# Kernel tuning notes

Measured on AMD Instinct MI355X. Metric: run time of the kernel, lower is better.

Reference implementation:

```python
import jax, jax.numpy as jnp
import numpy as np

N = 20000   # nodes
E = 320000  # edges
F0 = 32     # num_features
H = 8       # GAT heads
G = 64      # graphs in batch


def setup_inputs() -> dict:
    key = jax.random.key(0)
    ks = jax.random.split(key, 16)
    def p(k, shape, s=0.05):
        return jax.random.normal(k, shape, jnp.float32) * s
    d = {}
    d['x'] = jax.random.normal(ks[0], (N, F0), jnp.float32)
    d['edge_index'] = jax.random.randint(ks[1], (2, E), 0, N, dtype=jnp.int32)
    d['edge_weights'] = jax.random.uniform(ks[2], (E,), jnp.float32)
    d['batch'] = jnp.sort(jax.random.randint(ks[3], (N,), 0, G, dtype=jnp.int32))
    # GATConv(32 -> 32, heads=8)
    d['W_gat'] = p(ks[4], (F0, H * F0)); d['att_src'] = p(ks[5], (H, F0))
    d['att_dst'] = p(ks[6], (H, F0));    d['b_gat'] = jnp.zeros((H * F0,), jnp.float32)
    # residual Linear(256 -> 1024) (widened so the residual add is shape-consistent)
    d['W_res'] = p(ks[7], (H * F0, 1024)); d['b_res'] = jnp.zeros((1024,), jnp.float32)
    # GCNConv(256 -> 512) + BN1
    d['W2'] = p(ks[8], (H * F0, 512)); d['b2'] = jnp.zeros((512,), jnp.float32)
    d['g1'] = jnp.ones((512,), jnp.float32); d['be1'] = jnp.zeros((512,), jnp.float32)
    d['m1'] = jnp.zeros((512,), jnp.float32); d['v1'] = jnp.ones((512,), jnp.float32)
    # GCNConv(512 -> 1024) + BN2
    d['W3'] = p(ks[9], (512, 1024)); d['b3'] = jnp.zeros((1024,), jnp.float32)
    d['g2'] = jnp.ones((1024,), jnp.float32); d['be2'] = jnp.zeros((1024,), jnp.float32)
    d['m2'] = jnp.zeros((1024,), jnp.float32); d['v2'] = jnp.ones((1024,), jnp.float32)
    # head
    d['Wf1'] = p(ks[10], (1024, 256)); d['bf1'] = jnp.zeros((256,), jnp.float32)
    d['Wf2'] = p(ks[11], (256, 2));    d['bf2'] = jnp.zeros((2,), jnp.float32)
    return d


def _add_self_loops(edge_index, edge_weight, n):
    loop = jnp.arange(n, dtype=edge_index.dtype)
    ei = jnp.concatenate([edge_index, jnp.stack([loop, loop])], axis=1)
    ew = jnp.concatenate([edge_weight, jnp.ones((n,), edge_weight.dtype)])
    return ei, ew


def _gat(x, edge_index, W, att_src, att_dst, b, n):
    # PyG GATConv, concat=True, eval (attention dropout off). Self-loops already added.
    src, dst = edge_index[0], edge_index[1]
    h = (x @ W).reshape(n, H, -1)                    # [N,H,C]
    a_s = jnp.einsum('nhc,hc->nh', h, att_src)        # [N,H]
    a_d = jnp.einsum('nhc,hc->nh', h, att_dst)
    e = jax.nn.leaky_relu(a_s[src] + a_d[dst], 0.2)   # [E,H]
    m = jax.ops.segment_max(e, dst, num_segments=n)   # softmax over incoming edges
    ex = jnp.exp(e - m[dst])
    s = jax.ops.segment_sum(ex, dst, num_segments=n)
    alpha = ex / s[dst]
    out = jax.ops.segment_sum(h[src] * alpha[:, :, None], dst, num_segments=n)
    return out.reshape(n, -1) + b                     # [N,H*C]


def _gcn(x, edge_index, w, W, b, n):
    # PyG GCNConv with symmetric normalization; self-loops (weight 1) already added.
    src, dst = edge_index[0], edge_index[1]
    deg = jax.ops.segment_sum(w, dst, num_segments=n)
    dinv = jnp.where(deg > 0, jax.lax.rsqrt(jnp.maximum(deg, 1e-12)), 0.0)
    norm = dinv[src] * w * dinv[dst]                  # [E]
    h = x @ W                                         # transform first (cheaper)
    return jax.ops.segment_sum(h[src] * norm[:, None], dst, num_segments=n) + b


def _bn(x, g, b, m, v):
    return g * (x - m) * jax.lax.rsqrt(v + 1e-5) + b


def reference(x, edge_index, edge_weights, batch, W_gat, att_src, att_dst, b_gat,
              W_res, b_res, W2, b2, g1, be1, m1, v1, W3, b3, g2, be2, m2, v2,
              Wf1, bf1, Wf2, bf2):
    n = x.shape[0]
    ei, ew = _add_self_loops(edge_index, edge_weights, n)
    h = jax.nn.relu(_gat(x, ei, W_gat, att_src, att_dst, b_gat, n))   # [N,256]
    res = h @ W_res + b_res                                           # [N,1024]
    h = _gcn(h, ei, ew, W2, b2, n)                                    # [N,512]
    h = jax.nn.relu(_bn(h, g1, be1, m1, v1))
    h = _gcn(h, ei, ew, W3, b3, n)                                    # [N,1024]
    h = jax.nn.relu(_bn(h, g2, be2, m2, v2))
    h = h + res
    pooled = jax.ops.segment_max(h, batch, num_segments=G)            # global max pool [G,1024]
    z = jax.nn.relu(pooled @ Wf1 + bf1)                               # dropout is eval no-op
    return z @ Wf2 + bf2                                              # [G,2]
```

## Files before the change

### kernel.cpp

```cpp
#include <hip/hip_runtime.h>
#include <hip/hip_bf16.h>

#define NN 20000
#define EE 320000
#define GG 64
#define EN (EE + NN)
#define MT 157

typedef float f32x4 __attribute__((ext_vector_type(4)));
typedef __bf16 bf16x4 __attribute__((ext_vector_type(4)));
typedef __bf16 bf16x8 __attribute__((ext_vector_type(8)));

__device__ __forceinline__ void gl_lds16(const void* g, void* l) {
    __builtin_amdgcn_global_load_lds((const __attribute__((address_space(1))) void*)g,
                                     (__attribute__((address_space(3))) void*)l, 16, 0, 0);
}

__global__ void sentinel_kernel(float* out, int n) {
    int i = blockIdx.x * 256 + threadIdx.x;
    if (i < n) out[i] = 12345.0f;
}

__global__ void init_kernel(int* deg_cnt, float* deg_w, int* fill, float* pooled) {
    int i = blockIdx.x * 256 + threadIdx.x;
    if (i < NN) { deg_cnt[i] = 1; deg_w[i] = 1.0f; fill[i] = 0; }
    if (i < GG * 1024) pooled[i] = -INFINITY;
}

__global__ void deg_kernel(const int* __restrict__ ei, const float* __restrict__ ew,
                           int* deg_cnt, float* deg_w) {
    int e = blockIdx.x * 256 + threadIdx.x;
    if (e >= EE) return;
    int dst = ei[EE + e];
    atomicAdd(&deg_cnt[dst], 1);
    atomicAdd(&deg_w[dst], ew[e]);
}

__global__ __launch_bounds__(256) void scan_kernel(const int* __restrict__ deg_cnt, int* __restrict__ rowptr) {
    __shared__ int partial[256];
    int tid = threadIdx.x;
    const int chunk = (NN + 255) / 256;
    int s0 = tid * chunk, s1 = min(s0 + chunk, NN);
    int sum = 0;
    for (int i = s0; i < s1; i++) sum += deg_cnt[i];
    partial[tid] = sum;
    __syncthreads();
    if (tid == 0) {
        int run = 0;
        for (int i = 0; i < 256; i++) { int t = partial[i]; partial[i] = run; run += t; }
        rowptr[NN] = run;
    }
    __syncthreads();
    int run = partial[tid];
    for (int i = s0; i < s1; i++) { rowptr[i] = run; run += deg_cnt[i]; }
}

__global__ void fill_kernel(const int* __restrict__ ei, const float* __restrict__ ew,
                            const float* __restrict__ deg_w, const int* __restrict__ rowptr,
                            int* fill, int* __restrict__ csr_src, float* __restrict__ csr_norm) {
    int e = blockIdx.x * 256 + threadIdx.x;
    if (e >= EN) return;
    int src, dst; float w;
    if (e < EE) { src = ei[e]; dst = ei[EE + e]; w = ew[e]; }
    else        { src = dst = e - EE; w = 1.0f; }
    int pos = atomicAdd(&fill[dst], 1);
    int slot = rowptr[dst] + pos;
    csr_src[slot] = src;
    csr_norm[slot] = rsqrtf(deg_w[src]) * w * rsqrtf(deg_w[dst]);
}

__global__ __launch_bounds__(256) void convert_all(
    const float* __restrict__ W2, const float* __restrict__ W3, const float* __restrict__ Wres,
    __bf16* __restrict__ W2t, __bf16* __restrict__ W3t, __bf16* __restrict__ Wrt)
{
    __shared__ float tile[64][65];
    int b = blockIdx.x;
    const float* W; __bf16* Wt; int K, N, bx, by;
    if (b < 32)       { W = W2;   Wt = W2t; K = 256; N = 512;  int bb = b;       bx = bb & 7;  by = bb >> 3; }
    else if (b < 160) { W = W3;   Wt = W3t; K = 512; N = 1024; int bb = b - 32;  bx = bb & 15; by = bb >> 4; }
    else              { W = Wres; Wt = Wrt; K = 256; N = 1024; int bb = b - 160; bx = bb & 15; by = bb >> 4; }
    int kb = by * 64, nb = bx * 64;
    int tx = threadIdx.x & 63, ty = threadIdx.x >> 6;
#pragma unroll
    for (int i = ty; i < 64; i += 4)
        tile[i][tx] = W[(size_t)(kb + i) * N + nb + tx];
    __syncthreads();
#pragma unroll
    for (int i = ty; i < 64; i += 4)
        Wt[(size_t)(nb + i) * K + kb + tx] = (__bf16)tile[tx][i];
}


__global__ __launch_bounds__(256) void a_compute(
    const float* __restrict__ x, const float* __restrict__ W,
    const float* __restrict__ att_s, const float* __restrict__ att_d,
    float* __restrict__ a_s, float* __restrict__ a_d)
{
    __shared__ float wss[8][32], wsd[8][32];
    __shared__ float xs[32][33];
    int tid = threadIdx.x;
    {
        int h = tid >> 5, k = tid & 31;
        float s = 0.f, d = 0.f;
#pragma unroll
        for (int c = 0; c < 32; c++) {
            float wv = W[k * 256 + h * 32 + c];
            s += wv * att_s[h * 32 + c];
            d += wv * att_d[h * 32 + c];
        }
        wss[h][k] = s; wsd[h][k] = d;
    }
    __syncthreads();
    for (int n0 = blockIdx.x * 32; n0 < NN; n0 += gridDim.x * 32) {
#pragma unroll
        for (int i = 0; i < 4; i++) {
            int idx = tid + i * 256;
            xs[idx >> 5][idx & 31] = x[(size_t)n0 * 32 + idx];
        }
        __syncthreads();
        int nl = tid >> 3, h = tid & 7;
        float s = 0.f, d = 0.f;
#pragma unroll
        for (int k = 0; k < 32; k++) {
            float xv = xs[nl][k];
            s += xv * wss[h][k];
            d += xv * wsd[h][k];
        }
        a_s[(n0 + nl) * 8 + h] = s;
        a_d[(n0 + nl) * 8 + h] = d;
        __syncthreads();
    }
}

__global__ __launch_bounds__(256) void gat_agg_x(
    const int* __restrict__ rowptr, const int* __restrict__ csr_src,
    const float* __restrict__ a_s, const float* __restrict__ a_d,
    const float* __restrict__ x, __bf16* __restrict__ xagg)
{
    int widx = threadIdx.x >> 6, lane = threadIdx.x & 63;
    int node = blockIdx.x * 4 + widx;
    int base = rowptr[node], deg = rowptr[node + 1] - base;
    int hA = lane & 7, eslot = lane >> 3;
    int c = lane & 31, half = lane >> 5;
    float adA = a_d[node * 8 + hA];
    float acc0[4] = {}, acc1[4] = {};

    if (deg <= 64) {
        int sv = (lane < deg) ? csr_src[base + lane] : 0;
        float ev[8];
        float psum = 0.f;
#pragma unroll
        for (int j = 0; j < 8; j++) {
            int e = j * 8 + eslot;
            float v = 0.f;
            if (e < deg) {
                int src = __shfl(sv, e);
                float t = a_s[src * 8 + hA] + adA;
                t = (t > 0.f) ? t : 0.2f * t;
                v = __expf(t);
            }
            ev[j] = v;
            psum += v;
        }
#pragma unroll
        for (int m = 8; m <= 32; m <<= 1) psum += __shfl_xor(psum, m);
        float sinv[4];
#pragma unroll
        for (int jj = 0; jj < 4; jj++) sinv[jj] = 1.f / __shfl(psum, half * 4 + jj);
#pragma unroll
        for (int j = 0; j < 8; j++) {
            if (j * 8 >= deg) break;
            int lim = min(8, deg - j * 8);
            int t = 0;
            for (; t + 1 < lim; t += 2) {
                int srcA = __shfl(sv, j * 8 + t), srcB = __shfl(sv, j * 8 + t + 1);
                float xvA = x[(size_t)srcA * 32 + c];
                float xvB = x[(size_t)srcB * 32 + c];
#pragma unroll
                for (int jj = 0; jj < 4; jj++) {
                    float aA = __shfl(ev[j], (t << 3) | (half * 4 + jj)) * sinv[jj];
                    float aB = __shfl(ev[j], ((t + 1) << 3) | (half * 4 + jj)) * sinv[jj];
                    acc0[jj] += aA * xvA;
                    acc1[jj] += aB * xvB;
                }
            }
            if (t < lim) {
                int src = __shfl(sv, j * 8 + t);
                float xv = x[(size_t)src * 32 + c];
#pragma unroll
                for (int jj = 0; jj < 4; jj++) {
                    float a = __shfl(ev[j], (t << 3) | (half * 4 + jj)) * sinv[jj];
                    acc0[jj] += a * xv;
                }
            }
        }
    } else {
        float sum = 0.f;
        for (int e = 0; e < deg; e++) {
            int src = csr_src[base + e];
            float t = a_s[src * 8 + hA] + adA;
            t = (t > 0.f) ? t : 0.2f * t;
            sum += __expf(t);
        }
        float sinv[4], ad4[4];
#pragma unroll
        for (int jj = 0; jj < 4; jj++) {
            sinv[jj] = 1.f / __shfl(sum, half * 4 + jj);
            ad4[jj] = a_d[node * 8 + half * 4 + jj];
        }
        for (int e = 0; e < deg; e++) {
            int src = csr_src[base + e];
            float xv = x[(size_t)src * 32 + c];
#pragma unroll
            for (int jj = 0; jj < 4; jj++) {
                float t = a_s[src * 8 + half * 4 + jj] + ad4[jj];
                t = (t > 0.f) ? t : 0.2f * t;
                acc0[jj] += __expf(t) * sinv[jj] * xv;
            }
        }
    }
#pragma unroll
    for (int jj = 0; jj < 4; jj++)
        xagg[(size_t)node * 256 + (half * 4 + jj) * 32 + c] = (__bf16)(acc0[jj] + acc1[jj]);
}

__global__ __launch_bounds__(256) void gat_post(
    const __bf16* __restrict__ xagg, const float* __restrict__ W,
    const float* __restrict__ b_gat, __bf16* __restrict__ h1)
{
    __shared__ float Ws[32 * 256];
    __shared__ float xr[256];
    int tid = threadIdx.x;
#pragma unroll
    for (int k = 0; k < 32; k++) Ws[k * 256 + tid] = W[k * 256 + tid];
    float bg = b_gat[tid];
    int h = tid >> 5;
    __syncthreads();
    for (int n = blockIdx.x; n < NN; n += gridDim.x) {
        xr[tid] = (float)xagg[(size_t)n * 256 + tid];
        __syncthreads();
        float acc = 0.f;
#pragma unroll
        for (int k = 0; k < 32; k++) acc += xr[h * 32 + k] * Ws[k * 256 + tid];
        h1[(size_t)n * 256 + tid] = (__bf16)fmaxf(acc + bg, 0.f);
        __syncthreads();
    }
}

template <int C, int SPLIT>
__global__ __launch_bounds__(256) void gcn_agg(
    const int* __restrict__ rowptr, const int* __restrict__ csr_src,
    const float* __restrict__ csr_norm, const __bf16* __restrict__ feat,
    __bf16* __restrict__ out)
{
    constexpr int V = C / (64 * SPLIT);
    int widx = threadIdx.x >> 6, lane = threadIdx.x & 63;
    int node = blockIdx.x * (4 / SPLIT) + widx / SPLIT;
    int half = widx % SPLIT;
    int coff = half * (C / SPLIT) + lane * V;
    int base = rowptr[node], deg = rowptr[node + 1] - base;
    float acc0[V], acc1[V], acc2[V], acc3[V];
#pragma unroll
    for (int j = 0; j < V; j++) { acc0[j] = 0.f; acc1[j] = 0.f; acc2[j] = 0.f; acc3[j] = 0.f; }
    const __bf16* fb = feat + coff;
    typedef __bf16 bf16v __attribute__((ext_vector_type(V)));
    for (int e0 = 0; e0 < deg; e0 += 64) {
        int cnt = min(64, deg - e0);
        int sv = 0; float wv = 0.f;
        if (lane < cnt) { sv = csr_src[base + e0 + lane]; wv = csr_norm[base + e0 + lane]; }
        int s = 0;
        for (; s + 3 < cnt; s += 4) {
            int sA = __shfl(sv, s),     sB = __shfl(sv, s + 1);
            int sC = __shfl(sv, s + 2), sD = __shfl(sv, s + 3);
            float wA = __shfl(wv, s),     wB = __shfl(wv, s + 1);
            float wC = __shfl(wv, s + 2), wD = __shfl(wv, s + 3);
            bf16v fA = *(const bf16v*)(fb + (size_t)sA * C);
            bf16v fB = *(const bf16v*)(fb + (size_t)sB * C);
            bf16v fC = *(const bf16v*)(fb + (size_t)sC * C);
            bf16v fD = *(const bf16v*)(fb + (size_t)sD * C);
#pragma unroll
            for (int j = 0; j < V; j++) {
                acc0[j] += wA * (float)fA[j]; acc1[j] += wB * (float)fB[j];
                acc2[j] += wC * (float)fC[j]; acc3[j] += wD * (float)fD[j];
            }
        }
        for (; s < cnt; s++) {
            int src = __shfl(sv, s);
            float w = __shfl(wv, s);
            bf16v f = *(const bf16v*)(fb + (size_t)src * C);
#pragma unroll
            for (int j = 0; j < V; j++) acc0[j] += w * (float)f[j];
        }
    }
    bf16v o;
#pragma unroll
    for (int j = 0; j < V; j++) o[j] = (__bf16)((acc0[j] + acc1[j]) + (acc2[j] + acc3[j]));
    *(bf16v*)(out + (size_t)node * C + coff) = o;
}


__device__ __forceinline__ void stage_async64(
    const __bf16* __restrict__ A, int K, const __bf16* __restrict__ Wt,
    int bm, int bn, int k0, int tid, __bf16* As, __bf16* Bs)
{
#pragma unroll
    for (int i = 0; i < 4; i++) {
        int j = i * 256 + tid;
        int r = j >> 3, c = j & 7;
        const __bf16* gp = A + (size_t)(bm + r) * K + k0 + ((c ^ (r & 7)) * 8);
        gl_lds16(gp, As + (size_t)(j & ~63) * 8);
    }
#pragma unroll
    for (int i = 0; i < 4; i++) {
        int j = i * 256 + tid;
        int r = j >> 3, c = j & 7;
        const __bf16* gp = Wt + (size_t)(bn + r) * K + k0 + ((c ^ (r & 7)) * 8);
        gl_lds16(gp, Bs + (size_t)(j & ~63) * 8);
    }
}

__device__ __forceinline__ void mfma_step64(
    const __bf16* As, const __bf16* Bs, int wr, int wc, int l16, int q, f32x4 (&acc)[4][4])
{
#pragma unroll
    for (int ks = 0; ks < 2; ks++) {
        bf16x8 af[4], bfv[4];
#pragma unroll
        for (int mt = 0; mt < 4; mt++) {
            int row = wr * 64 + mt * 16 + l16;
            af[mt] = *(const bf16x8*)(As + row * 64 + (((ks * 4 + q) ^ (row & 7)) * 8));
        }
#pragma unroll
        for (int nt = 0; nt < 4; nt++) {
            int row = wc * 64 + nt * 16 + l16;
            bfv[nt] = *(const bf16x8*)(Bs + row * 64 + (((ks * 4 + q) ^ (row & 7)) * 8));
        }
#pragma unroll
        for (int mt = 0; mt < 4; mt++)
#pragma unroll
            for (int nt = 0; nt < 4; nt++)
                acc[mt][nt] = __builtin_amdgcn_mfma_f32_16x16x32_bf16(af[mt], bfv[nt], acc[mt][nt], 0, 0, 0);
    }
}

__device__ __forceinline__ void gemm_loop(
    const __bf16* __restrict__ A, int K, const __bf16* __restrict__ Wt,
    int bm, int bn, int tid, int wr, int wc, int l16, int q,
    __bf16* As, __bf16* Bs, f32x4 (&acc)[4][4])
{
    for (int k0 = 0; k0 < K; k0 += 64) {
        stage_async64(A, K, Wt, bm, bn, k0, tid, As, Bs);
        __syncthreads();
        mfma_step64(As, Bs, wr, wc, l16, q, acc);
        __syncthreads();
    }
}

__global__ __launch_bounds__(256) void gemm_bn_relu(
    const __bf16* __restrict__ A, const __bf16* __restrict__ Wt,
    int M, int K, int Nc,
    const float* __restrict__ bias,
    const float* __restrict__ g, const float* __restrict__ be,
    const float* __restrict__ mu, const float* __restrict__ var,
    __bf16* __restrict__ C)
{
    __shared__ __bf16 As[128 * 64];
    __shared__ __bf16 Bs[128 * 64];
    int tid = threadIdx.x;
    int w = tid >> 6, wr = w >> 1, wc = w & 1;
    int l = tid & 63, q = l >> 4, l16 = l & 15;
    int i = blockIdx.x;
    int k = (i & 3) * MT + (i >> 2);
    int bm = (k >> 2) * 128, bn = (k & 3) * 128;
    f32x4 acc[4][4] = {};
    gemm_loop(A, K, Wt, bm, bn, tid, wr, wc, l16, q, As, Bs, acc);
#pragma unroll
    for (int nt = 0; nt < 4; nt++) {
        int gn = bn + wc * 64 + nt * 16 + l16;
        float s = g[gn] * rsqrtf(var[gn] + 1e-5f);
        float t = be[gn] - mu[gn] * s;
        float bv = bias[gn];
#pragma unroll
        for (int mt = 0; mt < 4; mt++)
#pragma unroll
            for (int r = 0; r < 4; r++) {
                int gm = bm + wr * 64 + mt * 16 + q * 4 + r;
                if (gm < M) C[(size_t)gm * Nc + gn] = (__bf16)fmaxf((acc[mt][nt][r] + bv) * s + t, 0.f);
            }
    }
}

__device__ __forceinline__ void atomicMaxFloat(float* addr, float value) {
    if (value >= 0.f) atomicMax((int*)addr, __float_as_int(value));
    else              atomicMin((unsigned int*)addr, __float_as_uint(value));
}

__global__ __launch_bounds__(256) void gemm_final(
    const __bf16* __restrict__ A1, const __bf16* __restrict__ W3t,
    const __bf16* __restrict__ A2, const __bf16* __restrict__ Wrt,
    const float* __restrict__ b3, const float* __restrict__ bres,
    const float* __restrict__ g, const float* __restrict__ be,
    const float* __restrict__ mu, const float* __restrict__ var,
    const int* __restrict__ batch, float* __restrict__ pooled)
{
    const int M = NN;
    __shared__ __bf16 As[128 * 64];
    __shared__ __bf16 Bs[128 * 64];
    __shared__ int bat[128];
    int tid = threadIdx.x;
    int w = tid >> 6, wr = w >> 1, wc = w & 1;
    int l = tid & 63, q = l >> 4, l16 = l & 15;
    int i = blockIdx.x;
    int k = (i & 7) * MT + (i >> 3);
    int bm = (k >> 3) * 128, bn = (k & 7) * 128;
    if (tid < 128) bat[tid] = (bm + tid < M) ? batch[bm + tid] : -1;
    f32x4 acc[4][4] = {};
    f32x4 accR[4][4] = {};
    gemm_loop(A1, 512, W3t, bm, bn, tid, wr, wc, l16, q, As, Bs, acc);
    gemm_loop(A2, 256, Wrt, bm, bn, tid, wr, wc, l16, q, As, Bs, accR);
#pragma unroll
    for (int nt = 0; nt < 4; nt++) {
        int gn = bn + wc * 64 + nt * 16 + l16;
        float s = g[gn] * rsqrtf(var[gn] + 1e-5f);
        float t = be[gn] - mu[gn] * s;
        float bv3 = b3[gn];
        float bvr = bres[gn];
        int cb = -1; float run = 0.f;
#pragma unroll
        for (int mt = 0; mt < 4; mt++)
#pragma unroll
            for (int r = 0; r < 4; r++) {
                int lr = wr * 64 + mt * 16 + q * 4 + r;
                int id = bat[lr];
                if (id < 0) continue;
                float v = fmaxf((acc[mt][nt][r] + bv3) * s + t, 0.f) + accR[mt][nt][r] + bvr;
                if (id == cb) run = fmaxf(run, v);
                else {
                    if (cb >= 0) atomicMaxFloat(&pooled[cb * 1024 + gn], run);
                    cb = id; run = v;
                }
            }
        if (cb >= 0) atomicMaxFloat(&pooled[cb * 1024 + gn], run);
    }
}

__global__ __launch_bounds__(256) void head_kernel(
    const float* __restrict__ pooled, const float* __restrict__ Wf1, const float* __restrict__ bf1,
    const float* __restrict__ Wf2, const float* __restrict__ bf2, float* __restrict__ out)
{
    int gph = blockIdx.x, tid = threadIdx.x;
    __shared__ float prow[1024];
    __shared__ float zred[256];
    for (int i = tid; i < 1024; i += 256) prow[i] = pooled[gph * 1024 + i];
    __syncthreads();
    float z = 0.f;
    for (int k = 0; k < 1024; k++) z += prow[k] * Wf1[k * 256 + tid];
    z = fmaxf(z + bf1[tid], 0.f);
    for (int c = 0; c < 2; c++) {
        zred[tid] = z * Wf2[tid * 2 + c];
        __syncthreads();
        for (int s = 128; s > 0; s >>= 1) { if (tid < s) zred[tid] += zred[tid + s]; __syncthreads(); }
        if (tid == 0) out[gph * 2 + c] = zred[0] + bf2[c];
        __syncthreads();
    }
}

extern "C" void kernel_launch(void* const* d_in, const int* in_sizes, int n_in,
                              void* d_out, int out_size, void* d_ws, size_t ws_size,
                              hipStream_t stream) {
    const float* x       = (const float*)d_in[0];
    const int*   ei      = (const int*)d_in[1];
    const float* ew      = (const float*)d_in[2];
    const int*   batch   = (const int*)d_in[3];
    const float* W_gat   = (const float*)d_in[4];
    const float* att_src = (const float*)d_in[5];
    const float* att_dst = (const float*)d_in[6];
    const float* b_gat   = (const float*)d_in[7];
    const float* W_res   = (const float*)d_in[8];
    const float* b_res   = (const float*)d_in[9];
    const float* W2      = (const float*)d_in[10];
    const float* b2v     = (const float*)d_in[11];
    const float* g1      = (const float*)d_in[12];
    const float* be1     = (const float*)d_in[13];
    const float* m1      = (const float*)d_in[14];
    const float* v1      = (const float*)d_in[15];
    const float* W3      = (const float*)d_in[16];
    const float* b3      = (const float*)d_in[17];
    const float* g2      = (const float*)d_in[18];
    const float* be2     = (const float*)d_in[19];
    const float* m2      = (const float*)d_in[20];
    const float* v2      = (const float*)d_in[21];
    const float* Wf1     = (const float*)d_in[22];
    const float* bf1     = (const float*)d_in[23];
    const float* Wf2     = (const float*)d_in[24];
    const float* bf2v    = (const float*)d_in[25];
    float* out           = (float*)d_out;

    char* ws = (char*)d_ws;
    size_t off = 0;
    auto alloc = [&](size_t bytes) { size_t o = off; off += (bytes + 255) & ~(size_t)255; return o; };
    size_t o_hlin   = alloc((size_t)NN * 256 * 2);
    size_t o_h1     = alloc((size_t)NN * 256 * 2);
    size_t o_h2     = alloc((size_t)NN * 512 * 2);
    size_t o_agg2   = alloc((size_t)NN * 512 * 2);
    size_t o_as     = alloc((size_t)NN * 8 * 4);
    size_t o_ad     = alloc((size_t)NN * 8 * 4);
    size_t o_degc   = alloc((size_t)NN * 4);
    size_t o_degw   = alloc((size_t)NN * 4);
    size_t o_rowptr = alloc((size_t)(NN + 1) * 4);
    size_t o_fill   = alloc((size_t)NN * 4);
    size_t o_csrs   = alloc((size_t)EN * 4);
    size_t o_csrn   = alloc((size_t)EN * 4);
    size_t o_pool   = alloc((size_t)GG * 1024 * 4);
    size_t o_w2t    = alloc((size_t)512 * 256 * 2);
    size_t o_w3t    = alloc((size_t)1024 * 512 * 2);
    size_t o_wrt    = alloc((size_t)1024 * 256 * 2);
    if (off > ws_size) {
        sentinel_kernel<<<(out_size + 255) / 256, 256, 0, stream>>>(out, out_size);
        return;
    }

    __bf16* xagg   = (__bf16*)(ws + o_hlin);
    __bf16* agg1   = xagg;
    __bf16* h1     = (__bf16*)(ws + o_h1);
    __bf16* h2     = (__bf16*)(ws + o_h2);
    __bf16* agg2   = (__bf16*)(ws + o_agg2);
    float*  a_s    = (float*)(ws + o_as);
    float*  a_d    = (float*)(ws + o_ad);
    int*    degc   = (int*)(ws + o_degc);
    float*  degw   = (float*)(ws + o_degw);
    int*    rowptr = (int*)(ws + o_rowptr);
    int*    fillb  = (int*)(ws + o_fill);
    int*    csrs   = (int*)(ws + o_csrs);
    float*  csrn   = (float*)(ws + o_csrn);
    float*  pooled = (float*)(ws + o_pool);
    __bf16* W2t    = (__bf16*)(ws + o_w2t);
    __bf16* W3t    = (__bf16*)(ws + o_w3t);
    __bf16* Wrt    = (__bf16*)(ws + o_wrt);

    convert_all<<<224, 256, 0, stream>>>(W2, W3, W_res, W2t, W3t, Wrt);
    a_compute<<<128, 256, 0, stream>>>(x, W_gat, att_src, att_dst, a_s, a_d);

    init_kernel<<<256, 256, 0, stream>>>(degc, degw, fillb, pooled);
    deg_kernel<<<(EE + 255) / 256, 256, 0, stream>>>(ei, ew, degc, degw);
    scan_kernel<<<1, 256, 0, stream>>>(degc, rowptr);
    fill_kernel<<<(EN + 255) / 256, 256, 0, stream>>>(ei, ew, degw, rowptr, fillb, csrs, csrn);

    gat_agg_x<<<NN / 4, 256, 0, stream>>>(rowptr, csrs, a_s, a_d, x, xagg);
    gat_post<<<512, 256, 0, stream>>>(xagg, W_gat, b_gat, h1);

    gcn_agg<256, 1><<<NN / 4, 256, 0, stream>>>(rowptr, csrs, csrn, h1, agg1);
    gemm_bn_relu<<<4 * MT, 256, 0, stream>>>(agg1, W2t, NN, 256, 512, b2v,
        g1, be1, m1, v1, h2);
    gcn_agg<512, 2><<<NN / 2, 256, 0, stream>>>(rowptr, csrs, csrn, h2, agg2);
    gemm_final<<<8 * MT, 256, 0, stream>>>(agg2, W3t, h1, Wrt,
        b3, b_res, g2, be2, m2, v2, batch, pooled);

    head_kernel<<<GG, 256, 0, stream>>>(pooled, Wf1, bf1, Wf2, bf2v, out);
}
```

Baseline: 439.3 us.

## Parallelize degree scan across blocks and use wave shuffles in GAT post

The single-block serial prefix scan over 20000 degrees becomes a three-kernel scan: per-block reductions, a tiny serial top-level scan over 79 block sums, and a per-block Hillis-Steele scan that writes rowptr. gat_post now broadcasts the per-head input values with wave shuffles instead of staging them in LDS, which removes two block barriers per node, and its grid grows from 512 to 1280 blocks. The change aims to remove a serialized latency bottleneck and synchronization overhead, at the cost of two extra kernel launches.

New measurement: 421.6 us. 4.0% less time.

```diff
diff --git a/kernel.cpp b/kernel.cpp
--- a/kernel.cpp
+++ b/kernel.cpp
@@ -6,6 +6,7 @@
 #define GG 64
 #define EN (EE + NN)
 #define MT 157
+#define SB 79
 
 typedef float f32x4 __attribute__((ext_vector_type(4)));
 typedef __bf16 bf16x4 __attribute__((ext_vector_type(4)));
@@ -36,23 +37,37 @@
     atomicAdd(&deg_w[dst], ew[e]);
 }
 
-__global__ __launch_bounds__(256) void scan_kernel(const int* __restrict__ deg_cnt, int* __restrict__ rowptr) {
-    __shared__ int partial[256];
-    int tid = threadIdx.x;
-    const int chunk = (NN + 255) / 256;
-    int s0 = tid * chunk, s1 = min(s0 + chunk, NN);
-    int sum = 0;
-    for (int i = s0; i < s1; i++) sum += deg_cnt[i];
-    partial[tid] = sum;
+__global__ __launch_bounds__(256) void scan_blocks(const int* __restrict__ deg_cnt, int* __restrict__ bsum) {
+    __shared__ int red[256];
+    int tid = threadIdx.x, i = blockIdx.x * 256 + tid;
+    red[tid] = (i < NN) ? deg_cnt[i] : 0;
     __syncthreads();
-    if (tid == 0) {
+    for (int s = 128; s > 0; s >>= 1) { if (tid < s) red[tid] += red[tid + s]; __syncthreads(); }
+    if (tid == 0) bsum[blockIdx.x] = red[0];
+}
+
+__global__ void scan_top(int* __restrict__ bsum, int* __restrict__ rowptr) {
+    if (threadIdx.x == 0) {
         int run = 0;
-        for (int i = 0; i < 256; i++) { int t = partial[i]; partial[i] = run; run += t; }
+        for (int i = 0; i < SB; i++) { int t = bsum[i]; bsum[i] = run; run += t; }
         rowptr[NN] = run;
     }
+}
+
+__global__ __launch_bounds__(256) void scan_write(const int* __restrict__ deg_cnt,
+                                                  const int* __restrict__ bsum, int* __restrict__ rowptr) {
+    __shared__ int sc[256];
+    int tid = threadIdx.x, b = blockIdx.x, i = b * 256 + tid;
+    int v = (i < NN) ? deg_cnt[i] : 0;
+    sc[tid] = v;
     __syncthreads();
-    int run = partial[tid];
-    for (int i = s0; i < s1; i++) { rowptr[i] = run; run += deg_cnt[i]; }
+    for (int ofs = 1; ofs < 256; ofs <<= 1) {
+        int t = (tid >= ofs) ? sc[tid - ofs] : 0;
+        __syncthreads();
+        sc[tid] += t;
+        __syncthreads();
+    }
+    if (i < NN) rowptr[i] = bsum[b] + sc[tid] - v;
 }
 
 __global__ void fill_kernel(const int* __restrict__ ei, const float* __restrict__ ew,
@@ -229,21 +244,18 @@
     const float* __restrict__ b_gat, __bf16* __restrict__ h1)
 {
     __shared__ float Ws[32 * 256];
-    __shared__ float xr[256];
     int tid = threadIdx.x;
 #pragma unroll
     for (int k = 0; k < 32; k++) Ws[k * 256 + tid] = W[k * 256 + tid];
     float bg = b_gat[tid];
-    int h = tid >> 5;
+    int lbase = tid & 32;
     __syncthreads();
     for (int n = blockIdx.x; n < NN; n += gridDim.x) {
-        xr[tid] = (float)xagg[(size_t)n * 256 + tid];
-        __syncthreads();
+        float xv = (float)xagg[(size_t)n * 256 + tid];
         float acc = 0.f;
 #pragma unroll
-        for (int k = 0; k < 32; k++) acc += xr[h * 32 + k] * Ws[k * 256 + tid];
+        for (int k = 0; k < 32; k++) acc += __shfl(xv, lbase + k) * Ws[k * 256 + tid];
         h1[(size_t)n * 256 + tid] = (__bf16)fmaxf(acc + bg, 0.f);
-        __syncthreads();
     }
 }
 
@@ -509,6 +521,7 @@
     size_t o_degw   = alloc((size_t)NN * 4);
     size_t o_rowptr = alloc((size_t)(NN + 1) * 4);
     size_t o_fill   = alloc((size_t)NN * 4);
+    size_t o_bsum   = alloc((size_t)SB * 4);
     size_t o_csrs   = alloc((size_t)EN * 4);
     size_t o_csrn   = alloc((size_t)EN * 4);
     size_t o_pool   = alloc((size_t)GG * 1024 * 4);
@@ -531,6 +544,7 @@
     float*  degw   = (float*)(ws + o_degw);
     int*    rowptr = (int*)(ws + o_rowptr);
     int*    fillb  = (int*)(ws + o_fill);
+    int*    bsum   = (int*)(ws + o_bsum);
     int*    csrs   = (int*)(ws + o_csrs);
     float*  csrn   = (float*)(ws + o_csrn);
     float*  pooled = (float*)(ws + o_pool);
@@ -543,11 +557,13 @@
 
     init_kernel<<<256, 256, 0, stream>>>(degc, degw, fillb, pooled);
     deg_kernel<<<(EE + 255) / 256, 256, 0, stream>>>(ei, ew, degc, degw);
-    scan_kernel<<<1, 256, 0, stream>>>(degc, rowptr);
+    scan_blocks<<<SB, 256, 0, stream>>>(degc, bsum);
+    scan_top<<<1, 64, 0, stream>>>(bsum, rowptr);
+    scan_write<<<SB, 256, 0, stream>>>(degc, bsum, rowptr);
     fill_kernel<<<(EN + 255) / 256, 256, 0, stream>>>(ei, ew, degw, rowptr, fillb, csrs, csrn);
 
     gat_agg_x<<<NN / 4, 256, 0, stream>>>(rowptr, csrs, a_s, a_d, x, xagg);
-    gat_post<<<512, 256, 0, stream>>>(xagg, W_gat, b_gat, h1);
+    gat_post<<<1280, 256, 0, stream>>>(xagg, W_gat, b_gat, h1);
 
     gcn_agg<256, 1><<<NN / 4, 256, 0, stream>>>(rowptr, csrs, csrn, h1, agg1);
     gemm_bn_relu<<<4 * MT, 256, 0, stream>>>(agg1, W2t, NN, 256, 512, b2v,
```
